# Optimization experiments

Hardware: AMD Instinct MI355X
Metric: run time of the kernel (lower is better)

## Reference

```python
import jax, jax.numpy as jnp
import numpy as np

N_NODES = 100000
N_EDGES = 1600000
N_GRAPHS = 1024
F_NODE = 16
F_EDGE = 8
F_GRAPH = 10
F_OUT = 1
H = 64
EPS = 1e-7  # GENConv eps
T = 1.0     # GENConv softmax temperature (learn_t=False default)


def _lin_init(key, fi, fo):
    kw, kb = jax.random.split(key)
    s = 1.0 / np.sqrt(fi)
    W = jax.random.uniform(kw, (fi, fo), jnp.float32, -s, s)
    b = jax.random.uniform(kb, (fo,), jnp.float32, -s, s)
    return W, b


def setup_inputs() -> dict:
    key = jax.random.key(0)
    ks = jax.random.split(key, 24)
    inp = {
        'x': jax.random.normal(ks[0], (N_NODES, F_NODE), jnp.float32),
        'edge_attr': jax.random.normal(ks[1], (N_EDGES, F_EDGE), jnp.float32),
        'graph_attr': jax.random.normal(ks[2], (N_GRAPHS, F_GRAPH), jnp.float32),
        'edge_index': jax.random.randint(ks[3], (2, N_EDGES), 0, N_NODES),
        'batch': jnp.sort(jax.random.randint(ks[4], (N_NODES,), 0, N_GRAPHS)),
    }
    inp['node_W'], inp['node_b'] = _lin_init(ks[5], F_NODE, H)
    inp['edge_W'], inp['edge_b'] = _lin_init(ks[6], F_EDGE, H)
    # three GENConv MLPs: Linear(H,2H) -> BN(identity @eval) -> ReLU -> Linear(2H,H)
    for i, k1, k2 in ((1, ks[7], ks[8]), (2, ks[9], ks[10]), (3, ks[11], ks[12])):
        inp[f'c{i}_W1'], inp[f'c{i}_b1'] = _lin_init(k1, H, 2 * H)
        inp[f'c{i}_W2'], inp[f'c{i}_b2'] = _lin_init(k2, 2 * H, H)
    inp['d1_W'], inp['d1_b'] = _lin_init(ks[13], H + F_GRAPH, 32)
    inp['d2_W'], inp['d2_b'] = _lin_init(ks[14], 32, 32)
    inp['out_W'], inp['out_b'] = _lin_init(ks[15], 32, F_OUT)
    return inp


def _genconv(h, src, dst, ea, W1, b1, W2, b2):
    # message: relu(x_j + edge_attr) + eps   [E, H]
    msg = jax.nn.relu(h[src] + ea) + EPS
    # per-destination, per-feature segment softmax (aggr='softmax', t=1)
    m = jax.ops.segment_max(msg * T, dst, num_segments=N_NODES)   # [N, H]
    e = jnp.exp(msg * T - m[dst])                                  # [E, H]
    denom = jax.ops.segment_sum(e, dst, num_segments=N_NODES)     # [N, H]
    alpha = e / jnp.maximum(denom[dst], 1e-16)
    agg = jax.ops.segment_sum(msg * alpha, dst, num_segments=N_NODES)
    out = h + agg  # root add
    # MLP (BatchNorm is identity in eval with default stats)
    hid = jax.nn.relu(out @ W1 + b1)
    return hid @ W2 + b2


def reference(x, edge_attr, graph_attr, node_W, node_b, edge_W, edge_b,
              c1_W1, c1_b1, c1_W2, c1_b2,
              c2_W1, c2_b1, c2_W2, c2_b2,
              c3_W1, c3_b1, c3_W2, c3_b2,
              d1_W, d1_b, d2_W, d2_b, out_W, out_b,
              edge_index, batch):
    src, dst = edge_index[0], edge_index[1]
    h = x @ node_W + node_b
    ea = edge_attr @ edge_W + edge_b
    h = jax.nn.relu(_genconv(h, src, dst, ea, c1_W1, c1_b1, c1_W2, c1_b2))
    h = jax.nn.relu(_genconv(h, src, dst, ea, c2_W1, c2_b1, c2_W2, c2_b2))
    h = jax.nn.relu(_genconv(h, src, dst, ea, c3_W1, c3_b1, c3_W2, c3_b2))
    # global mean pool over graphs
    sums = jax.ops.segment_sum(h, batch, num_segments=N_GRAPHS)          # [G, H]
    cnt = jax.ops.segment_sum(jnp.ones((h.shape[0],), h.dtype), batch, num_segments=N_GRAPHS)
    pooled = sums / jnp.maximum(cnt, 1.0)[:, None]
    g = jnp.concatenate([pooled, graph_attr], axis=1)                    # [G, H+F_GRAPH]
    g = jax.nn.relu(g @ d1_W + d1_b)   # dropout = identity at eval
    g = jax.nn.relu(g @ d2_W + d2_b)
    return jax.nn.sigmoid(g @ out_W + out_b)                             # [G, 1]
```

## Files before the change

### kernel.cpp

```cpp
#include <hip/hip_runtime.h>
#include <hip/hip_bf16.h>

#define N_NODES 100000
#define N_EDGES 1600000
#define N_GRAPHS 1024
#define F_NODE 16
#define F_EDGE 8
#define F_GRAPH 10
#define HD 64
#define HD2 128
#define GEN_EPS 1e-7f
#define SCAN_NBLK ((N_NODES + 255) / 256)

typedef unsigned short u16;
typedef unsigned int u32;
typedef __attribute__((ext_vector_type(8))) short short8;
typedef __attribute__((ext_vector_type(4))) float floatx4;

__device__ __forceinline__ u16 f2bf(float x) {
    u32 u = __float_as_uint(x);
    return (u16)((u + 0x7FFFu + ((u >> 16) & 1u)) >> 16);
}
__device__ __forceinline__ float bf2f(u16 u) {
    return __uint_as_float(((u32)u) << 16);
}

__global__ void __launch_bounds__(256) k_node_embed(
        const float* __restrict__ x, const float* __restrict__ W,
        const float* __restrict__ b, float* __restrict__ h,
        u16* __restrict__ hb) {
    __shared__ float sW[F_NODE * HD];
    __shared__ float sb[HD];
    for (int i = threadIdx.x; i < F_NODE * HD; i += 256) sW[i] = W[i];
    if (threadIdx.x < HD) sb[threadIdx.x] = b[threadIdx.x];
    __syncthreads();
    int t = blockIdx.x * 256 + threadIdx.x;
    if (t >= N_NODES * HD) return;
    int n = t >> 6, f = t & 63;
    const float* xr = x + (size_t)n * F_NODE;
    float acc = sb[f];
#pragma unroll
    for (int k = 0; k < F_NODE; k++) acc += xr[k] * sW[k * HD + f];
    h[t] = acc;
    hb[t] = f2bf(acc);
}

__global__ void __launch_bounds__(256) k_hist(
        const int* __restrict__ dst, int* __restrict__ deg,
        int* __restrict__ rank) {
    int e = blockIdx.x * 256 + threadIdx.x;
    if (e >= N_EDGES) return;
    rank[e] = atomicAdd(&deg[dst[e]], 1);
}

__global__ void __launch_bounds__(256) k_scan1(
        const int* __restrict__ deg, int* __restrict__ bsum) {
    __shared__ int red[256];
    int t = threadIdx.x;
    int g = blockIdx.x * 256 + t;
    red[t] = (g < N_NODES) ? deg[g] : 0;
    __syncthreads();
    for (int s = 128; s > 0; s >>= 1) {
        if (t < s) red[t] += red[t + s];
        __syncthreads();
    }
    if (t == 0) bsum[blockIdx.x] = red[0];
}

__global__ void __launch_bounds__(512) k_scan2(
        const int* __restrict__ bsum, int* __restrict__ bpre) {
    __shared__ int sh[512];
    int t = threadIdx.x;
    int v = (t < SCAN_NBLK) ? bsum[t] : 0;
    sh[t] = v;
    __syncthreads();
    for (int d = 1; d < 512; d <<= 1) {
        int u = (t >= d) ? sh[t - d] : 0;
        __syncthreads();
        sh[t] += u;
        __syncthreads();
    }
    if (t < SCAN_NBLK) bpre[t] = sh[t] - v;
}

__global__ void __launch_bounds__(256) k_scan3(
        const int* __restrict__ deg, const int* __restrict__ bpre,
        int* __restrict__ off) {
    __shared__ int sh[256];
    int t = threadIdx.x;
    int g = blockIdx.x * 256 + t;
    int v = (g < N_NODES) ? deg[g] : 0;
    sh[t] = v;
    __syncthreads();
    for (int d = 1; d < 256; d <<= 1) {
        int u = (t >= d) ? sh[t - d] : 0;
        __syncthreads();
        sh[t] += u;
        __syncthreads();
    }
    int incl = sh[t];
    int base = bpre[blockIdx.x];
    if (g < N_NODES) off[g] = base + incl - v;
    if (g == N_NODES - 1) off[N_NODES] = base + incl;
}

__global__ void __launch_bounds__(256) k_scatter(
        const int* __restrict__ src, const int* __restrict__ dst,
        const int* __restrict__ rank, const int* __restrict__ off,
        const float* __restrict__ eattr,
        unsigned int* __restrict__ rec) {
    int e = blockIdx.x * 256 + threadIdx.x;
    if (e >= N_EDGES) return;
    const uint4* ap = reinterpret_cast<const uint4*>(eattr + (size_t)e * F_EDGE);
    uint4 a0 = ap[0], a1 = ap[1];
    unsigned int s = (unsigned int)src[e];
    a0.x = (a0.x & ~7u) | (s & 7u);
    a0.y = (a0.y & ~7u) | ((s >> 3) & 7u);
    a0.z = (a0.z & ~7u) | ((s >> 6) & 7u);
    a0.w = (a0.w & ~7u) | ((s >> 9) & 7u);
    a1.x = (a1.x & ~7u) | ((s >> 12) & 7u);
    a1.y = (a1.y & ~7u) | ((s >> 15) & 3u);
    int pos = off[dst[e]] + rank[e];
    uint4* op = reinterpret_cast<uint4*>(rec + (size_t)pos * 8);
    op[0] = a0;
    op[1] = a1;
}

__device__ __forceinline__ float u2f(unsigned int u) {
    return __uint_as_float(u);
}

__global__ void __launch_bounds__(256) k_gen_agg(
        const float* __restrict__ h, const u16* __restrict__ hb,
        const int* __restrict__ off,
        const unsigned int* __restrict__ rec,
        const float* __restrict__ eW, const float* __restrict__ eb,
        float* __restrict__ outb) {
    int n = blockIdx.x * 4 + (threadIdx.x >> 6);
    if (n >= N_NODES) return;
    int f = threadIdx.x & 63;
    float w[F_EDGE];
#pragma unroll
    for (int k = 0; k < F_EDGE; k++) w[k] = eW[k * HD + f];
    float bf = eb[f];
    int nu = __builtin_amdgcn_readfirstlane(n);
    int beg = off[nu], end = off[nu + 1];
    float den = 0.f, nm = 0.f;
    int i = beg;
    for (; i + 8 <= end; i += 8) {
        uint4 q0[8], q1[8];
#pragma unroll
        for (int u = 0; u < 8; u++) {
            const uint4* rp = reinterpret_cast<const uint4*>(
                rec + (size_t)(i + u) * 8);
            q0[u] = rp[0];
            q1[u] = rp[1];
        }
        int s[8];
#pragma unroll
        for (int u = 0; u < 8; u++) {
            s[u] = (int)((q0[u].x & 7u) | ((q0[u].y & 7u) << 3)
                       | ((q0[u].z & 7u) << 6) | ((q0[u].w & 7u) << 9)
                       | ((q1[u].x & 7u) << 12) | ((q1[u].y & 3u) << 15));
        }
        float hv[8];
#pragma unroll
        for (int u = 0; u < 8; u++) hv[u] = bf2f(hb[(size_t)s[u] * HD + f]);
#pragma unroll
        for (int u = 0; u < 8; u++) {
            float ea = bf + u2f(q0[u].x) * w[0] + u2f(q0[u].y) * w[1]
                          + u2f(q0[u].z) * w[2] + u2f(q0[u].w) * w[3]
                          + u2f(q1[u].x) * w[4] + u2f(q1[u].y) * w[5]
                          + u2f(q1[u].z) * w[6] + u2f(q1[u].w) * w[7];
            float m = fmaxf(hv[u] + ea, 0.f) + GEN_EPS;
            float ev = __expf(m);
            den += ev;
            nm += m * ev;
        }
    }
    for (; i < end; i++) {
        const uint4* rp = reinterpret_cast<const uint4*>(rec + (size_t)i * 8);
        uint4 q0 = rp[0], q1 = rp[1];
        int s = (int)((q0.x & 7u) | ((q0.y & 7u) << 3)
                    | ((q0.z & 7u) << 6) | ((q0.w & 7u) << 9)
                    | ((q1.x & 7u) << 12) | ((q1.y & 3u) << 15));
        float hv = bf2f(hb[(size_t)s * HD + f]);
        float ea = bf + u2f(q0.x) * w[0] + u2f(q0.y) * w[1]
                      + u2f(q0.z) * w[2] + u2f(q0.w) * w[3]
                      + u2f(q1.x) * w[4] + u2f(q1.y) * w[5]
                      + u2f(q1.z) * w[6] + u2f(q1.w) * w[7];
        float m = fmaxf(hv + ea, 0.f) + GEN_EPS;
        float ev = __expf(m);
        den += ev;
        nm += m * ev;
    }
    size_t idx = (size_t)n * HD + f;
    outb[idx] = h[idx] + nm / fmaxf(den, 1e-16f);
}

__global__ void __launch_bounds__(256) k_mlp1(
        const float* __restrict__ inb,
        const float* __restrict__ W1, const float* __restrict__ b1,
        u16* __restrict__ hid) {
    __shared__ u16 wB[HD2][HD + 8];
    __shared__ float sb1[HD2];
    int tid = threadIdx.x;
    for (int i = tid; i < HD * HD2; i += 256) {
        int f = i >> 7, j = i & 127;
        wB[j][f] = f2bf(W1[i]);
    }
    if (tid < HD2) sb1[tid] = b1[tid];
    __syncthreads();
    int wid = tid >> 6, lane = tid & 63;
    int quad = lane >> 4, lm = lane & 15;
    int n0 = blockIdx.x * 64 + wid * 16;
    if (n0 >= N_NODES) return;
    int node = n0 + lm;
    short8 a[2];
    const float* ar = inb + (size_t)node * HD;
#pragma unroll
    for (int kk = 0; kk < 2; kk++) {
        const float4* p = reinterpret_cast<const float4*>(ar + kk * 32 + quad * 8);
        float4 v0 = p[0], v1 = p[1];
        short8 t;
        t[0] = (short)f2bf(v0.x); t[1] = (short)f2bf(v0.y);
        t[2] = (short)f2bf(v0.z); t[3] = (short)f2bf(v0.w);
        t[4] = (short)f2bf(v1.x); t[5] = (short)f2bf(v1.y);
        t[6] = (short)f2bf(v1.z); t[7] = (short)f2bf(v1.w);
        a[kk] = t;
    }
#pragma unroll
    for (int jt = 0; jt < 8; jt++) {
        int jb = jt * 16;
        float bias = sb1[jb + lm];
        floatx4 acc = {bias, bias, bias, bias};
#pragma unroll
        for (int kk = 0; kk < 2; kk++) {
            const short8* bp = reinterpret_cast<const short8*>(
                &wB[jb + lm][kk * 32 + quad * 8]);
            acc = __builtin_amdgcn_mfma_f32_16x16x32_bf16(a[kk], *bp, acc, 0, 0, 0);
        }
#pragma unroll
        for (int r = 0; r < 4; r++) {
            int orow = n0 + quad * 4 + r;
            hid[(size_t)orow * HD2 + jb + lm] = f2bf(fmaxf(acc[r], 0.f));
        }
    }
}

__global__ void __launch_bounds__(256) k_mlp2(
        const u16* __restrict__ hid,
        const float* __restrict__ W2, const float* __restrict__ b2,
        float* __restrict__ hout, u16* __restrict__ hbout) {
    __shared__ u16 wB[HD][HD2 + 8];
    __shared__ float sb2[HD];
    int tid = threadIdx.x;
    for (int i = tid; i < HD2 * HD; i += 256) {
        int j = i >> 6, c = i & 63;
        wB[c][j] = f2bf(W2[i]);
    }
    if (tid < HD) sb2[tid] = b2[tid];
    __syncthreads();
    int wid = tid >> 6, lane = tid & 63;
    int quad = lane >> 4, lm = lane & 15;
    int n0 = blockIdx.x * 64 + wid * 16;
    if (n0 >= N_NODES) return;
    int node = n0 + lm;
    short8 a[4];
    const u16* ar = hid + (size_t)node * HD2;
#pragma unroll
    for (int kk = 0; kk < 4; kk++)
        a[kk] = *reinterpret_cast<const short8*>(ar + kk * 32 + quad * 8);
#pragma unroll
    for (int ct = 0; ct < 4; ct++) {
        int cb = ct * 16;
        float bias = sb2[cb + lm];
        floatx4 acc = {bias, bias, bias, bias};
#pragma unroll
        for (int kk = 0; kk < 4; kk++) {
            const short8* bp = reinterpret_cast<const short8*>(
                &wB[cb + lm][kk * 32 + quad * 8]);
            acc = __builtin_amdgcn_mfma_f32_16x16x32_bf16(a[kk], *bp, acc, 0, 0, 0);
        }
#pragma unroll
        for (int r = 0; r < 4; r++) {
            int orow = n0 + quad * 4 + r;
            float o = fmaxf(acc[r], 0.f);
            hout[(size_t)orow * HD + cb + lm] = o;
            hbout[(size_t)orow * HD + cb + lm] = f2bf(o);
        }
    }
}

__global__ void __launch_bounds__(256) k_pool(
        const float* __restrict__ h, const int* __restrict__ batch,
        float* __restrict__ pooled) {
    int g = blockIdx.x * 4 + (threadIdx.x >> 6);
    if (g >= N_GRAPHS) return;
    int f = threadIdx.x & 63;
    int lo = 0, hi = N_NODES;
    while (lo < hi) {
        int mid = (lo + hi) >> 1;
        if (batch[mid] < g) lo = mid + 1; else hi = mid;
    }
    int b = lo;
    int lo2 = b, hi2 = N_NODES;
    while (lo2 < hi2) {
        int mid = (lo2 + hi2) >> 1;
        if (batch[mid] < g + 1) lo2 = mid + 1; else hi2 = mid;
    }
    int e = lo2;
    float s = 0.f;
    for (int n = b; n < e; n++) s += h[(size_t)n * HD + f];
    float cnt = fmaxf((float)(e - b), 1.f);
    pooled[(size_t)g * HD + f] = s / cnt;
}

__global__ void __launch_bounds__(64) k_head(
        const float* __restrict__ pooled, const float* __restrict__ gattr,
        const float* __restrict__ d1W, const float* __restrict__ d1b,
        const float* __restrict__ d2W, const float* __restrict__ d2b,
        const float* __restrict__ oW, const float* __restrict__ ob,
        float* __restrict__ out) {
    int g = blockIdx.x;
    __shared__ float si[HD + F_GRAPH];
    __shared__ float s1[32], s2[32];
    int t = threadIdx.x;
    if (t < HD) si[t] = pooled[(size_t)g * HD + t];
    if (t < F_GRAPH) si[HD + t] = gattr[(size_t)g * F_GRAPH + t];
    __syncthreads();
    if (t < 32) {
        float acc = d1b[t];
        for (int i = 0; i < HD + F_GRAPH; i++) acc += si[i] * d1W[i * 32 + t];
        s1[t] = fmaxf(acc, 0.f);
    }
    __syncthreads();
    if (t < 32) {
        float acc = d2b[t];
        for (int i = 0; i < 32; i++) acc += s1[i] * d2W[i * 32 + t];
        s2[t] = fmaxf(acc, 0.f);
    }
    __syncthreads();
    if (t == 0) {
        float acc = ob[0];
        for (int i = 0; i < 32; i++) acc += s2[i] * oW[i];
        out[g] = 1.f / (1.f + __expf(-acc));
    }
}

extern "C" void kernel_launch(void* const* d_in, const int* in_sizes, int n_in,
                              void* d_out, int out_size, void* d_ws, size_t ws_size,
                              hipStream_t stream) {
    const float* x     = (const float*)d_in[0];
    const float* eattr = (const float*)d_in[1];
    const float* gattr = (const float*)d_in[2];
    const int*   eidx  = (const int*)d_in[3];
    const int*   batch = (const int*)d_in[4];
    const float* nodeW = (const float*)d_in[5];
    const float* nodeb = (const float*)d_in[6];
    const float* edgeW = (const float*)d_in[7];
    const float* edgeb = (const float*)d_in[8];
    const float* cW1[3] = {(const float*)d_in[9],  (const float*)d_in[13], (const float*)d_in[17]};
    const float* cb1[3] = {(const float*)d_in[10], (const float*)d_in[14], (const float*)d_in[18]};
    const float* cW2[3] = {(const float*)d_in[11], (const float*)d_in[15], (const float*)d_in[19]};
    const float* cb2[3] = {(const float*)d_in[12], (const float*)d_in[16], (const float*)d_in[20]};
    const float* d1W = (const float*)d_in[21];
    const float* d1b = (const float*)d_in[22];
    const float* d2W = (const float*)d_in[23];
    const float* d2b = (const float*)d_in[24];
    const float* oW  = (const float*)d_in[25];
    const float* ob  = (const float*)d_in[26];

    const int* src = eidx;
    const int* dst = eidx + N_EDGES;

    char* p = (char*)d_ws;
    float* h      = (float*)p; p += (size_t)N_NODES * HD * 4;
    float* outb   = (float*)p; p += (size_t)N_NODES * HD * 4;
    u16*   hid    = (u16*)p;   p += (size_t)N_NODES * HD2 * 2;
    unsigned int* rec = (unsigned int*)p; p += (size_t)N_EDGES * F_EDGE * 4;
    u16*   hb     = (u16*)p;   p += (size_t)N_NODES * HD * 2;
    float* pooled = (float*)p; p += (size_t)N_GRAPHS * HD * 4;
    int*   off    = (int*)p;   p += (size_t)(N_NODES + 1) * 4;
    int*   deg    = (int*)p;   p += (size_t)N_NODES * 4;
    int*   rank   = (int*)p;   p += (size_t)N_EDGES * 4;
    int*   bsum   = (int*)p;   p += (size_t)(SCAN_NBLK + 1) * 4;
    int*   bpre   = (int*)p;   p += (size_t)(SCAN_NBLK + 1) * 4;

    const int EB = (N_EDGES + 255) / 256;
    const int NBM = (N_NODES + 63) / 64;

    k_node_embed<<<(N_NODES * HD + 255) / 256, 256, 0, stream>>>(x, nodeW, nodeb, h, hb);

    hipMemsetAsync(deg, 0, (size_t)N_NODES * 4, stream);
    k_hist<<<EB, 256, 0, stream>>>(dst, deg, rank);
    k_scan1<<<SCAN_NBLK, 256, 0, stream>>>(deg, bsum);
    k_scan2<<<1, 512, 0, stream>>>(bsum, bpre);
    k_scan3<<<SCAN_NBLK, 256, 0, stream>>>(deg, bpre, off);
    k_scatter<<<EB, 256, 0, stream>>>(src, dst, rank, off, eattr, rec);

    for (int l = 0; l < 3; l++) {
        k_gen_agg<<<(N_NODES + 3) / 4, 256, 0, stream>>>(
            h, hb, off, rec, edgeW, edgeb, outb);
        k_mlp1<<<NBM, 256, 0, stream>>>(outb, cW1[l], cb1[l], hid);
        k_mlp2<<<NBM, 256, 0, stream>>>(hid, cW2[l], cb2[l], h, hb);
    }

    k_pool<<<(N_GRAPHS + 3) / 4, 256, 0, stream>>>(h, batch, pooled);
    k_head<<<N_GRAPHS, 64, 0, stream>>>(pooled, gattr,
                                        d1W, d1b, d2W, d2b, oW, ob,
                                        (float*)d_out);
}
```

Baseline: 737.8 us.

## Fuse MLP layers, store exact src indices, persistent-grid aggregation

Merges the two per-layer MLP kernels into one, keeping the 128-wide hidden activations in shared memory instead of a global bf16 buffer. Stores source indices in a separate array instead of packing them into the low bits of edge attributes. This restores exact attributes but adds a 4-byte load per edge. The aggregation kernel becomes a grid-stride loop over 2048 blocks, and the eps is moved out of the exponent and added once after the division, with zero-degree nodes handled. The fused MLP uses much more shared memory per block, which may lower occupancy.

```diff
diff --git a/kernel.cpp b/kernel.cpp
--- a/kernel.cpp
+++ b/kernel.cpp
@@ -24,6 +24,9 @@
 __device__ __forceinline__ float bf2f(u16 u) {
     return __uint_as_float(((u32)u) << 16);
 }
+__device__ __forceinline__ float u2f(unsigned int u) {
+    return __uint_as_float(u);
+}
 
 __global__ void __launch_bounds__(256) k_node_embed(
         const float* __restrict__ x, const float* __restrict__ W,
@@ -108,186 +111,169 @@
         const int* __restrict__ src, const int* __restrict__ dst,
         const int* __restrict__ rank, const int* __restrict__ off,
         const float* __restrict__ eattr,
-        unsigned int* __restrict__ rec) {
+        unsigned int* __restrict__ rec, int* __restrict__ srcs) {
     int e = blockIdx.x * 256 + threadIdx.x;
     if (e >= N_EDGES) return;
     const uint4* ap = reinterpret_cast<const uint4*>(eattr + (size_t)e * F_EDGE);
     uint4 a0 = ap[0], a1 = ap[1];
-    unsigned int s = (unsigned int)src[e];
-    a0.x = (a0.x & ~7u) | (s & 7u);
-    a0.y = (a0.y & ~7u) | ((s >> 3) & 7u);
-    a0.z = (a0.z & ~7u) | ((s >> 6) & 7u);
-    a0.w = (a0.w & ~7u) | ((s >> 9) & 7u);
-    a1.x = (a1.x & ~7u) | ((s >> 12) & 7u);
-    a1.y = (a1.y & ~7u) | ((s >> 15) & 3u);
     int pos = off[dst[e]] + rank[e];
     uint4* op = reinterpret_cast<uint4*>(rec + (size_t)pos * 8);
     op[0] = a0;
     op[1] = a1;
-}
-
-__device__ __forceinline__ float u2f(unsigned int u) {
-    return __uint_as_float(u);
+    srcs[pos] = src[e];
 }
 
 __global__ void __launch_bounds__(256) k_gen_agg(
         const float* __restrict__ h, const u16* __restrict__ hb,
         const int* __restrict__ off,
         const unsigned int* __restrict__ rec,
+        const int* __restrict__ srcs,
         const float* __restrict__ eW, const float* __restrict__ eb,
         float* __restrict__ outb) {
-    int n = blockIdx.x * 4 + (threadIdx.x >> 6);
-    if (n >= N_NODES) return;
     int f = threadIdx.x & 63;
     float w[F_EDGE];
 #pragma unroll
     for (int k = 0; k < F_EDGE; k++) w[k] = eW[k * HD + f];
     float bf = eb[f];
-    int nu = __builtin_amdgcn_readfirstlane(n);
-    int beg = off[nu], end = off[nu + 1];
-    float den = 0.f, nm = 0.f;
-    int i = beg;
-    for (; i + 8 <= end; i += 8) {
-        uint4 q0[8], q1[8];
-#pragma unroll
-        for (int u = 0; u < 8; u++) {
-            const uint4* rp = reinterpret_cast<const uint4*>(
-                rec + (size_t)(i + u) * 8);
-            q0[u] = rp[0];
-            q1[u] = rp[1];
-        }
-        int s[8];
-#pragma unroll
-        for (int u = 0; u < 8; u++) {
-            s[u] = (int)((q0[u].x & 7u) | ((q0[u].y & 7u) << 3)
-                       | ((q0[u].z & 7u) << 6) | ((q0[u].w & 7u) << 9)
-                       | ((q1[u].x & 7u) << 12) | ((q1[u].y & 3u) << 15));
-        }
-        float hv[8];
-#pragma unroll
-        for (int u = 0; u < 8; u++) hv[u] = bf2f(hb[(size_t)s[u] * HD + f]);
-#pragma unroll
-        for (int u = 0; u < 8; u++) {
-            float ea = bf + u2f(q0[u].x) * w[0] + u2f(q0[u].y) * w[1]
-                          + u2f(q0[u].z) * w[2] + u2f(q0[u].w) * w[3]
-                          + u2f(q1[u].x) * w[4] + u2f(q1[u].y) * w[5]
-                          + u2f(q1[u].z) * w[6] + u2f(q1[u].w) * w[7];
-            float m = fmaxf(hv[u] + ea, 0.f) + GEN_EPS;
-            float ev = __expf(m);
+    int wave0 = blockIdx.x * 4 + (threadIdx.x >> 6);
+    const int NW = gridDim.x * 4;
+    for (int n0 = wave0; n0 < N_NODES; n0 += NW) {
+        int n = __builtin_amdgcn_readfirstlane(n0);
+        int beg = off[n], end = off[n + 1];
+        size_t idx = (size_t)n * HD + f;
+        float hroot = h[idx];
+        float den = 0.f, nm = 0.f;
+        int i = beg;
+        for (; i + 8 <= end; i += 8) {
+            uint4 q0[8], q1[8];
+#pragma unroll
+            for (int u = 0; u < 8; u++) {
+                const uint4* rp = reinterpret_cast<const uint4*>(
+                    rec + (size_t)(i + u) * 8);
+                q0[u] = rp[0];
+                q1[u] = rp[1];
+            }
+            int s[8];
+#pragma unroll
+            for (int u = 0; u < 8; u++) s[u] = srcs[i + u];
+            float hv[8];
+#pragma unroll
+            for (int u = 0; u < 8; u++) hv[u] = bf2f(hb[(size_t)s[u] * HD + f]);
+#pragma unroll
+            for (int u = 0; u < 8; u++) {
+                float ea = bf + u2f(q0[u].x) * w[0] + u2f(q0[u].y) * w[1]
+                              + u2f(q0[u].z) * w[2] + u2f(q0[u].w) * w[3]
+                              + u2f(q1[u].x) * w[4] + u2f(q1[u].y) * w[5]
+                              + u2f(q1[u].z) * w[6] + u2f(q1[u].w) * w[7];
+                float r = fmaxf(hv[u] + ea, 0.f);
+                float ev = __expf(r);
+                den += ev;
+                nm += r * ev;
+            }
+        }
+        for (; i < end; i++) {
+            const uint4* rp = reinterpret_cast<const uint4*>(rec + (size_t)i * 8);
+            uint4 q0 = rp[0], q1 = rp[1];
+            int s = srcs[i];
+            float hv = bf2f(hb[(size_t)s * HD + f]);
+            float ea = bf + u2f(q0.x) * w[0] + u2f(q0.y) * w[1]
+                          + u2f(q0.z) * w[2] + u2f(q0.w) * w[3]
+                          + u2f(q1.x) * w[4] + u2f(q1.y) * w[5]
+                          + u2f(q1.z) * w[6] + u2f(q1.w) * w[7];
+            float r = fmaxf(hv + ea, 0.f);
+            float ev = __expf(r);
             den += ev;
-            nm += m * ev;
-        }
-    }
-    for (; i < end; i++) {
-        const uint4* rp = reinterpret_cast<const uint4*>(rec + (size_t)i * 8);
-        uint4 q0 = rp[0], q1 = rp[1];
-        int s = (int)((q0.x & 7u) | ((q0.y & 7u) << 3)
-                    | ((q0.z & 7u) << 6) | ((q0.w & 7u) << 9)
-                    | ((q1.x & 7u) << 12) | ((q1.y & 3u) << 15));
-        float hv = bf2f(hb[(size_t)s * HD + f]);
-        float ea = bf + u2f(q0.x) * w[0] + u2f(q0.y) * w[1]
-                      + u2f(q0.z) * w[2] + u2f(q0.w) * w[3]
-                      + u2f(q1.x) * w[4] + u2f(q1.y) * w[5]
-                      + u2f(q1.z) * w[6] + u2f(q1.w) * w[7];
-        float m = fmaxf(hv + ea, 0.f) + GEN_EPS;
-        float ev = __expf(m);
-        den += ev;
-        nm += m * ev;
-    }
-    size_t idx = (size_t)n * HD + f;
-    outb[idx] = h[idx] + nm / fmaxf(den, 1e-16f);
-}
-
-__global__ void __launch_bounds__(256) k_mlp1(
+            nm += r * ev;
+        }
+        float agg = (end > beg) ? (nm / fmaxf(den, 1e-16f) + GEN_EPS) : 0.f;
+        outb[idx] = hroot + agg;
+    }
+}
+
+__global__ void __launch_bounds__(256) k_mlp(
         const float* __restrict__ inb,
         const float* __restrict__ W1, const float* __restrict__ b1,
-        u16* __restrict__ hid) {
-    __shared__ u16 wB[HD2][HD + 8];
+        const float* __restrict__ W2, const float* __restrict__ b2,
+        float* __restrict__ hout, u16* __restrict__ hbout) {
+    __shared__ u16 wB1[HD2][HD + 8];
+    __shared__ u16 wB2[HD][HD2 + 8];
+    __shared__ u16 sHid[64][HD2 + 8];
     __shared__ float sb1[HD2];
+    __shared__ float sb2[HD];
     int tid = threadIdx.x;
     for (int i = tid; i < HD * HD2; i += 256) {
         int f = i >> 7, j = i & 127;
-        wB[j][f] = f2bf(W1[i]);
+        wB1[j][f] = f2bf(W1[i]);
+    }
+    for (int i = tid; i < HD2 * HD; i += 256) {
+        int j = i >> 6, c = i & 63;
+        wB2[c][j] = f2bf(W2[i]);
     }
     if (tid < HD2) sb1[tid] = b1[tid];
+    if (tid < HD) sb2[tid] = b2[tid];
     __syncthreads();
     int wid = tid >> 6, lane = tid & 63;
     int quad = lane >> 4, lm = lane & 15;
     int n0 = blockIdx.x * 64 + wid * 16;
-    if (n0 >= N_NODES) return;
-    int node = n0 + lm;
-    short8 a[2];
-    const float* ar = inb + (size_t)node * HD;
-#pragma unroll
-    for (int kk = 0; kk < 2; kk++) {
-        const float4* p = reinterpret_cast<const float4*>(ar + kk * 32 + quad * 8);
-        float4 v0 = p[0], v1 = p[1];
-        short8 t;
-        t[0] = (short)f2bf(v0.x); t[1] = (short)f2bf(v0.y);
-        t[2] = (short)f2bf(v0.z); t[3] = (short)f2bf(v0.w);
-        t[4] = (short)f2bf(v1.x); t[5] = (short)f2bf(v1.y);
-        t[6] = (short)f2bf(v1.z); t[7] = (short)f2bf(v1.w);
-        a[kk] = t;
-    }
-#pragma unroll
-    for (int jt = 0; jt < 8; jt++) {
-        int jb = jt * 16;
-        float bias = sb1[jb + lm];
-        floatx4 acc = {bias, bias, bias, bias};
+    bool active = (n0 < N_NODES);
+    if (active) {
+        int node = n0 + lm;
+        short8 a[2];
+        const float* ar = inb + (size_t)node * HD;
 #pragma unroll
         for (int kk = 0; kk < 2; kk++) {
-            const short8* bp = reinterpret_cast<const short8*>(
-                &wB[jb + lm][kk * 32 + quad * 8]);
-            acc = __builtin_amdgcn_mfma_f32_16x16x32_bf16(a[kk], *bp, acc, 0, 0, 0);
-        }
-#pragma unroll
-        for (int r = 0; r < 4; r++) {
-            int orow = n0 + quad * 4 + r;
-            hid[(size_t)orow * HD2 + jb + lm] = f2bf(fmaxf(acc[r], 0.f));
-        }
-    }
-}
-
-__global__ void __launch_bounds__(256) k_mlp2(
-        const u16* __restrict__ hid,
-        const float* __restrict__ W2, const float* __restrict__ b2,
-        float* __restrict__ hout, u16* __restrict__ hbout) {
-    __shared__ u16 wB[HD][HD2 + 8];
-    __shared__ float sb2[HD];
-    int tid = threadIdx.x;
-    for (int i = tid; i < HD2 * HD; i += 256) {
-        int j = i >> 6, c = i & 63;
-        wB[c][j] = f2bf(W2[i]);
-    }
-    if (tid < HD) sb2[tid] = b2[tid];
-    __syncthreads();
-    int wid = tid >> 6, lane = tid & 63;
-    int quad = lane >> 4, lm = lane & 15;
-    int n0 = blockIdx.x * 64 + wid * 16;
-    if (n0 >= N_NODES) return;
-    int node = n0 + lm;
-    short8 a[4];
-    const u16* ar = hid + (size_t)node * HD2;
-#pragma unroll
-    for (int kk = 0; kk < 4; kk++)
-        a[kk] = *reinterpret_cast<const short8*>(ar + kk * 32 + quad * 8);
-#pragma unroll
-    for (int ct = 0; ct < 4; ct++) {
-        int cb = ct * 16;
-        float bias = sb2[cb + lm];
-        floatx4 acc = {bias, bias, bias, bias};
-#pragma unroll
-        for (int kk = 0; kk < 4; kk++) {
-            const short8* bp = reinterpret_cast<const short8*>(
-                &wB[cb + lm][kk * 32 + quad * 8]);
-            acc = __builtin_amdgcn_mfma_f32_16x16x32_bf16(a[kk], *bp, acc, 0, 0, 0);
-        }
-#pragma unroll
-        for (int r = 0; r < 4; r++) {
-            int orow = n0 + quad * 4 + r;
-            float o = fmaxf(acc[r], 0.f);
-            hout[(size_t)orow * HD + cb + lm] = o;
-            hbout[(size_t)orow * HD + cb + lm] = f2bf(o);
+            const float4* p = reinterpret_cast<const float4*>(ar + kk * 32 + quad * 8);
+            float4 v0 = p[0], v1 = p[1];
+            short8 t;
+            t[0] = (short)f2bf(v0.x); t[1] = (short)f2bf(v0.y);
+            t[2] = (short)f2bf(v0.z); t[3] = (short)f2bf(v0.w);
+            t[4] = (short)f2bf(v1.x); t[5] = (short)f2bf(v1.y);
+            t[6] = (short)f2bf(v1.z); t[7] = (short)f2bf(v1.w);
+            a[kk] = t;
+        }
+#pragma unroll
+        for (int jt = 0; jt < 8; jt++) {
+            int jb = jt * 16;
+            float bias = sb1[jb + lm];
+            floatx4 acc = {bias, bias, bias, bias};
+#pragma unroll
+            for (int kk = 0; kk < 2; kk++) {
+                const short8* bp = reinterpret_cast<const short8*>(
+                    &wB1[jb + lm][kk * 32 + quad * 8]);
+                acc = __builtin_amdgcn_mfma_f32_16x16x32_bf16(a[kk], *bp, acc, 0, 0, 0);
+            }
+#pragma unroll
+            for (int r = 0; r < 4; r++) {
+                int lr = wid * 16 + quad * 4 + r;
+                sHid[lr][jb + lm] = f2bf(fmaxf(acc[r], 0.f));
+            }
+        }
+    }
+    __syncthreads();
+    if (active) {
+        short8 a2[4];
+#pragma unroll
+        for (int kk = 0; kk < 4; kk++)
+            a2[kk] = *reinterpret_cast<const short8*>(
+                &sHid[wid * 16 + lm][kk * 32 + quad * 8]);
+#pragma unroll
+        for (int ct = 0; ct < 4; ct++) {
+            int cb = ct * 16;
+            float bias = sb2[cb + lm];
+            floatx4 acc = {bias, bias, bias, bias};
+#pragma unroll
+            for (int kk = 0; kk < 4; kk++) {
+                const short8* bp = reinterpret_cast<const short8*>(
+                    &wB2[cb + lm][kk * 32 + quad * 8]);
+                acc = __builtin_amdgcn_mfma_f32_16x16x32_bf16(a2[kk], *bp, acc, 0, 0, 0);
+            }
+#pragma unroll
+            for (int r = 0; r < 4; r++) {
+                int orow = n0 + quad * 4 + r;
+                float o = fmaxf(acc[r], 0.f);
+                hout[(size_t)orow * HD + cb + lm] = o;
+                hbout[(size_t)orow * HD + cb + lm] = f2bf(o);
+            }
         }
     }
 }
@@ -377,7 +363,7 @@
     char* p = (char*)d_ws;
     float* h      = (float*)p; p += (size_t)N_NODES * HD * 4;
     float* outb   = (float*)p; p += (size_t)N_NODES * HD * 4;
-    u16*   hid    = (u16*)p;   p += (size_t)N_NODES * HD2 * 2;
+    int*   srcs   = (int*)p;   p += (size_t)N_EDGES * 4;
     unsigned int* rec = (unsigned int*)p; p += (size_t)N_EDGES * F_EDGE * 4;
     u16*   hb     = (u16*)p;   p += (size_t)N_NODES * HD * 2;
     float* pooled = (float*)p; p += (size_t)N_GRAPHS * HD * 4;
@@ -397,13 +383,12 @@
     k_scan1<<<SCAN_NBLK, 256, 0, stream>>>(deg, bsum);
     k_scan2<<<1, 512, 0, stream>>>(bsum, bpre);
     k_scan3<<<SCAN_NBLK, 256, 0, stream>>>(deg, bpre, off);
-    k_scatter<<<EB, 256, 0, stream>>>(src, dst, rank, off, eattr, rec);
+    k_scatter<<<EB, 256, 0, stream>>>(src, dst, rank, off, eattr, rec, srcs);
 
     for (int l = 0; l < 3; l++) {
-        k_gen_agg<<<(N_NODES + 3) / 4, 256, 0, stream>>>(
-            h, hb, off, rec, edgeW, edgeb, outb);
-        k_mlp1<<<NBM, 256, 0, stream>>>(outb, cW1[l], cb1[l], hid);
-        k_mlp2<<<NBM, 256, 0, stream>>>(hid, cW2[l], cb2[l], h, hb);
+        k_gen_agg<<<2048, 256, 0, stream>>>(
+            h, hb, off, rec, srcs, edgeW, edgeb, outb);
+        k_mlp<<<NBM, 256, 0, stream>>>(outb, cW1[l], cb1[l], cW2[l], cb2[l], h, hb);
     }
 
     k_pool<<<(N_GRAPHS + 3) / 4, 256, 0, stream>>>(h, batch, pooled);
```

Result: faster. 716.7 us (-2.9%).
